# Kernel tuning notes

Measured on AMD Instinct MI355X. Metric: run time of the kernel, lower is better.

Reference implementation:

```python
import jax, jax.numpy as jnp
import numpy as np

DIM = 512
NUM_HEADS = 8
HEAD_DIM = DIM // NUM_HEADS
B, S = 2, 2048


def setup_inputs() -> dict:
    key = jax.random.key(0)
    ks = jax.random.split(key, 16)
    scale = 1.0 / np.sqrt(DIM)
    inp = {
        "x": jax.random.normal(ks[0], (B, S, DIM), dtype=jnp.float32),
        "Qexpl": jax.random.normal(ks[1], (B, S, DIM), dtype=jnp.float32),
        "Kexpl": jax.random.normal(ks[2], (B, S, DIM), dtype=jnp.float32),
        "fl": jax.random.uniform(ks[3], (B,), dtype=jnp.float32),
        "fu": jax.random.uniform(ks[4], (B,), dtype=jnp.float32),
        "age": jax.random.uniform(ks[5], (B,), dtype=jnp.float32),
        "gender": jax.random.uniform(ks[6], (B,), dtype=jnp.float32),
        # Linear params: weight stored as [out, in] like torch; y = x @ W.T + b
        "Wq": jax.random.normal(ks[7], (DIM, DIM), dtype=jnp.float32) * scale,
        "bq": jnp.zeros((DIM,), dtype=jnp.float32),
        "Wk": jax.random.normal(ks[8], (DIM, DIM), dtype=jnp.float32) * scale,
        "bk": jnp.zeros((DIM,), dtype=jnp.float32),
        "Wv": jax.random.normal(ks[9], (DIM, DIM), dtype=jnp.float32) * scale,
        "bv": jnp.zeros((DIM,), dtype=jnp.float32),
        "Wo": jax.random.normal(ks[10], (DIM, DIM), dtype=jnp.float32) * scale,
        "bo": jnp.zeros((DIM,), dtype=jnp.float32),
    }
    return inp


def reference(x, Qexpl, Kexpl, fl, fu, age, gender, Wq, bq, Wk, bk, Wv, bv, Wo, bo):
    # drofe_fn is None -> Q/K projections used directly.
    Q = Qexpl @ Wq.T + bq            # [B, S, D]
    K = Kexpl @ Wk.T + bk            # [B, S, D]
    V = x @ Wv.T + bv                # [B, S, D]

    def split_heads(t):  # [B, S, D] -> [B, H, S, hd]
        return t.reshape(B, S, NUM_HEADS, HEAD_DIM).transpose(0, 2, 1, 3)

    Qh, Kh, Vh = split_heads(Q), split_heads(K), split_heads(V)
    scale = 1.0 / np.sqrt(HEAD_DIM).astype(np.float32)
    scores = jnp.einsum("bhqd,bhkd->bhqk", Qh, Kh) * scale  # [B, H, S, S]
    weights = jax.nn.softmax(scores, axis=-1)
    attn = jnp.einsum("bhqk,bhkd->bhqd", weights, Vh)        # [B, H, S, hd]
    attn = attn.transpose(0, 2, 1, 3).reshape(B, S, DIM)
    return attn @ Wo.T + bo
```

## Files before the change

### kernel.cpp

```cpp
#include <hip/hip_runtime.h>
#include <hip/hip_bf16.h>

typedef unsigned short ushort_t;
typedef __attribute__((ext_vector_type(8))) short bf16x8;
typedef __attribute__((ext_vector_type(4))) float f32x4;

__device__ __forceinline__ ushort_t f2bf(float f) {
    union { float f; unsigned u; } v; v.f = f;
    unsigned r = v.u + 0x7FFF + ((v.u >> 16) & 1);
    return (ushort_t)(r >> 16);
}
__device__ __forceinline__ float bfl(ushort_t u) {
    union { unsigned u; float f; } v; v.u = (unsigned)u << 16; return v.f;
}
__device__ __forceinline__ bf16x8 ld8(const ushort_t* p) { return *(const bf16x8*)p; }

__device__ __forceinline__ unsigned cvt2(float x, float y) {
    __hip_bfloat162 h = __float22bfloat162_rn(make_float2(x, y));
    unsigned r; __builtin_memcpy(&r, &h, 4); return r;
}
__device__ __forceinline__ bf16x8 pack8f(float4 a, float4 b) {
    union { unsigned u[4]; bf16x8 v; } o;
    o.u[0] = cvt2(a.x, a.y); o.u[1] = cvt2(a.z, a.w);
    o.u[2] = cvt2(b.x, b.y); o.u[3] = cvt2(b.z, b.w);
    return o.v;
}

__device__ __forceinline__ void gload_lds16(const ushort_t* g, ushort_t* l) {
    __builtin_amdgcn_global_load_lds(
        (const __attribute__((address_space(1))) void*)g,
        (__attribute__((address_space(3))) void*)l, 16, 0, 0);
}

__global__ __launch_bounds__(256)
void cast_kernel(const float* __restrict__ Qe, const float* __restrict__ Ke,
                 const float* __restrict__ x,  const float* __restrict__ Wq,
                 const float* __restrict__ Wk, const float* __restrict__ Wv,
                 const float* __restrict__ Wo,
                 ushort_t* __restrict__ Ab, ushort_t* __restrict__ Wb)
{
    const unsigned i8 = (blockIdx.x * 256u + threadIdx.x) * 8u;
    const float* src; ushort_t* dst;
    if (i8 < (3u << 21)) {
        unsigned a = i8 >> 21, off = i8 & ((1u << 21) - 1);
        src = (a == 0 ? Qe : a == 1 ? Ke : x) + off;
        dst = Ab + i8;
    } else {
        unsigned j = i8 - (3u << 21);
        unsigned a = j >> 18, off = j & ((1u << 18) - 1);
        src = (a == 0 ? Wq : a == 1 ? Wk : a == 2 ? Wv : Wo) + off;
        dst = Wb + j;
    }
    *(bf16x8*)dst = pack8f(*(const float4*)src, *(const float4*)(src + 4));
}

__global__ __launch_bounds__(256, 2)
void proj_qkv_kernel(const ushort_t* __restrict__ Ab, const ushort_t* __restrict__ Wb,
                     const float* __restrict__ bq, const float* __restrict__ bk,
                     const float* __restrict__ bv,
                     ushort_t* __restrict__ Qo, ushort_t* __restrict__ Ko,
                     ushort_t* __restrict__ Vt)
{
    __shared__ ushort_t smem[4 * 128 * 64];

    const int z = blockIdx.z;
    const ushort_t* A = Ab + ((size_t)z << 21);
    const ushort_t* W = Wb + ((size_t)z << 18);
    const float* bias = (z == 0) ? bq : (z == 1) ? bk : bv;

    const int m0 = blockIdx.y * 128, n0 = blockIdx.x * 128;
    const int t = threadIdx.x;
    const int lane = t & 63, wave = t >> 6;
    const int wm = (wave & 1) * 64, wn = (wave >> 1) * 64;
    const int fr = lane & 15, quad = lane >> 4;
    const int fr7 = fr & 7;

    const int srl = wave * 32 + (lane >> 3);
    const int sch = ((lane & 7) ^ (srl & 7)) << 3;
    const ushort_t* ag = A + (size_t)(m0 + srl) * 512 + sch;
    const ushort_t* wg = W + (size_t)(n0 + srl) * 512 + sch;
    const int dbase = wave * 32 * 64;

    f32x4 acc[4][4] = {};

#pragma unroll
    for (int i = 0; i < 4; ++i)
        gload_lds16(ag + (size_t)(i * 8) * 512, smem + dbase + i * 512);
#pragma unroll
    for (int i = 0; i < 4; ++i)
        gload_lds16(wg + (size_t)(i * 8) * 512, smem + 8192 + dbase + i * 512);
    __syncthreads();

    for (int kk = 0; kk < 8; ++kk) {
        ushort_t* cur = smem + ((kk & 1) << 14);
        ushort_t* nxt = smem + (((kk & 1) ^ 1) << 14);
        if (kk < 7) {
            int ko = (kk + 1) * 64;
#pragma unroll
            for (int i = 0; i < 4; ++i)
                gload_lds16(ag + ko + (size_t)(i * 8) * 512, nxt + dbase + i * 512);
#pragma unroll
            for (int i = 0; i < 4; ++i)
                gload_lds16(wg + ko + (size_t)(i * 8) * 512, nxt + 8192 + dbase + i * 512);
        }

#pragma unroll
        for (int ks = 0; ks < 2; ++ks) {
            bf16x8 af[4], bfr[4];
#pragma unroll
            for (int mt = 0; mt < 4; ++mt)
                af[mt] = ld8(cur + (wm + mt * 16 + fr) * 64 + (((ks * 4 + quad) ^ fr7) << 3));
#pragma unroll
            for (int nt = 0; nt < 4; ++nt)
                bfr[nt] = ld8(cur + 8192 + (wn + nt * 16 + fr) * 64 + (((ks * 4 + quad) ^ fr7) << 3));
#pragma unroll
            for (int mt = 0; mt < 4; ++mt)
#pragma unroll
                for (int nt = 0; nt < 4; ++nt)
                    acc[mt][nt] = __builtin_amdgcn_mfma_f32_16x16x32_bf16(
                        af[mt], bfr[nt], acc[mt][nt], 0, 0, 0);
        }
        asm volatile("s_waitcnt vmcnt(0)" ::: "memory");
        __builtin_amdgcn_s_barrier();
        __builtin_amdgcn_sched_barrier(0);
    }

    const float C1 = 0.125f * 1.44269504088896340736f;
    if (z != 2) {
        ushort_t* dst = (z == 0) ? Qo : Ko;
#pragma unroll
        for (int nt = 0; nt < 4; ++nt) {
            int n = n0 + wn + nt * 16 + fr;
            float bb = bias[n];
#pragma unroll
            for (int mt = 0; mt < 4; ++mt) {
                int mb = m0 + wm + mt * 16 + quad * 4;
                if (z == 0) {
#pragma unroll
                    for (int r = 0; r < 4; ++r)
                        dst[(size_t)(mb + r) * 512 + n] = f2bf((acc[mt][nt][r] + bb) * C1);
                } else {
#pragma unroll
                    for (int r = 0; r < 4; ++r)
                        dst[(size_t)(mb + r) * 512 + n] = f2bf(acc[mt][nt][r] + bb);
                }
            }
        }
    } else {
        ushort_t* lT = smem;
#pragma unroll
        for (int nt = 0; nt < 4; ++nt) {
            int nl = wn + nt * 16 + fr;
            float bb = bias[n0 + nl];
#pragma unroll
            for (int mt = 0; mt < 4; ++mt) {
                int tm = wm + mt * 16 + quad * 4;
#pragma unroll
                for (int r = 0; r < 4; ++r) {
                    int tl = tm + r;
                    int sg = (tl & 96) + ((tl & 12) << 1) + ((tl >> 4 & 1) << 2) + (tl & 3);
                    lT[nl * 136 + sg] = f2bf(acc[mt][nt][r] + bb);
                }
            }
        }
        __syncthreads();
        const int bidx = m0 >> 11, m0t = m0 & 2047;
#pragma unroll
        for (int i = 0; i < 8; ++i) {
            int s = i * 256 + t;
            int row = s >> 4, c = s & 15;
            int n = n0 + row;
            int h = n >> 6, d = n & 63;
            bf16x8 v = ld8(lT + row * 136 + c * 8);
            *(bf16x8*)(Vt + ((size_t)((bidx * 8 + h) * 64 + d)) * 2048 + m0t + c * 8) = v;
        }
    }
}

__global__ __launch_bounds__(256, 2)
void gemm_o_kernel(const ushort_t* __restrict__ Oh, const float* __restrict__ Lsum,
                   const ushort_t* __restrict__ W, const float* __restrict__ bias,
                   float* __restrict__ dst)
{
    __shared__ ushort_t lA[64 * 72];
    __shared__ ushort_t lB[64 * 72];
    const int m0 = blockIdx.y * 64, n0 = blockIdx.x * 64;
    const int t = threadIdx.x;
    const int lane = t & 63, wave = t >> 6;
    const int wm = (wave & 1) * 32, wn = (wave >> 1) * 32;
    const int fr = lane & 15, quad = lane >> 4;
    const int bq_ = m0 >> 11, qq0 = m0 & 2047;

    f32x4 acc[2][2] = {};
    bf16x8 va0[2], va1[2], vw[2];
    float l0[2], l1[2];

#pragma unroll
    for (int i = 0; i < 2; ++i) {
        int s = i * 256 + t;
        int r = s >> 3, jp = s & 7;
        va0[i] = ld8(Oh + (size_t)(m0 + r) * 512 + jp * 8);
        va1[i] = ld8(Oh + (size_t)(m0 + r + 4096) * 512 + jp * 8);
        l0[i] = Lsum[(bq_ * 8 + 0) * 2048 + qq0 + r];
        l1[i] = Lsum[((2 + bq_) * 8 + 0) * 2048 + qq0 + r];
        vw[i] = ld8(W + (size_t)(n0 + r) * 512 + jp * 8);
    }

    for (int kk = 0; kk < 8; ++kk) {
        if (kk) __syncthreads();
#pragma unroll
        for (int i = 0; i < 2; ++i) {
            int s = i * 256 + t;
            int r = s >> 3, jp = s & 7;
            float inv = 1.f / (l0[i] + l1[i]);
            union { bf16x8 v; ushort_t s8[8]; } a0, a1;
            a0.v = va0[i]; a1.v = va1[i];
            union { unsigned u[4]; bf16x8 v; } o;
#pragma unroll
            for (int j = 0; j < 4; ++j)
                o.u[j] = cvt2((bfl(a0.s8[2 * j]) + bfl(a1.s8[2 * j])) * inv,
                              (bfl(a0.s8[2 * j + 1]) + bfl(a1.s8[2 * j + 1])) * inv);
            *(bf16x8*)(lA + r * 72 + jp * 8) = o.v;
            *(bf16x8*)(lB + r * 72 + jp * 8) = vw[i];
        }
        __syncthreads();
        if (kk < 7) {
            int k0 = (kk + 1) * 64;
#pragma unroll
            for (int i = 0; i < 2; ++i) {
                int s = i * 256 + t;
                int r = s >> 3, jp = s & 7;
                va0[i] = ld8(Oh + (size_t)(m0 + r) * 512 + k0 + jp * 8);
                va1[i] = ld8(Oh + (size_t)(m0 + r + 4096) * 512 + k0 + jp * 8);
                l0[i] = Lsum[(bq_ * 8 + kk + 1) * 2048 + qq0 + r];
                l1[i] = Lsum[((2 + bq_) * 8 + kk + 1) * 2048 + qq0 + r];
                vw[i] = ld8(W + (size_t)(n0 + r) * 512 + k0 + jp * 8);
            }
        }

        bf16x8 af[2][2], bfrag[2][2];
#pragma unroll
        for (int ks = 0; ks < 2; ++ks) {
#pragma unroll
            for (int mt = 0; mt < 2; ++mt)
                af[mt][ks] = ld8(lA + (wm + mt * 16 + fr) * 72 + (ks * 4 + quad) * 8);
#pragma unroll
            for (int nt = 0; nt < 2; ++nt)
                bfrag[nt][ks] = ld8(lB + (wn + nt * 16 + fr) * 72 + (ks * 4 + quad) * 8);
        }
#pragma unroll
        for (int ks = 0; ks < 2; ++ks)
#pragma unroll
            for (int mt = 0; mt < 2; ++mt)
#pragma unroll
                for (int nt = 0; nt < 2; ++nt)
                    acc[mt][nt] = __builtin_amdgcn_mfma_f32_16x16x32_bf16(
                        af[mt][ks], bfrag[nt][ks], acc[mt][nt], 0, 0, 0);
    }

#pragma unroll
    for (int nt = 0; nt < 2; ++nt) {
        int n = n0 + wn + nt * 16 + fr;
        float bb = bias[n];
#pragma unroll
        for (int mt = 0; mt < 2; ++mt) {
            int mb = m0 + wm + mt * 16 + quad * 4;
#pragma unroll
            for (int r = 0; r < 4; ++r)
                dst[(size_t)(mb + r) * 512 + n] = acc[mt][nt][r] + bb;
        }
    }
}

__global__ __launch_bounds__(256, 4)
void attn_kernel(const ushort_t* __restrict__ Q, const ushort_t* __restrict__ K,
                 const ushort_t* __restrict__ Vt, ushort_t* __restrict__ Opart,
                 float* __restrict__ Lsum)
{
    __shared__ ushort_t lK[128 * 64];
    __shared__ ushort_t lV[64 * 128];

    const int b = blockIdx.z >> 1, half = blockIdx.z & 1;
    const int h = blockIdx.y;
    const int q0 = blockIdx.x * 64;
    const int kvbase = half * 1024;
    const int t = threadIdx.x;
    const int lane = t & 63, w = t >> 6;
    const int wq = w * 16;
    const int fr = lane & 15, quad = lane >> 4;
    const int fr7 = fr & 7;

    bf16x8 aq[2];
    {
        const ushort_t* qp = Q + (size_t)(b * 2048 + q0 + wq + fr) * 512 + h * 64 + quad * 8;
        aq[0] = ld8(qp);
        aq[1] = ld8(qp + 32);
    }

    const int krl = w * 32 + (lane >> 3);
    const ushort_t* kg = K + (size_t)(b * 2048 + kvbase + krl) * 512 + h * 64
                           + (lane & 7) * 8;
    ushort_t* lk_wr = lK + krl * 64 + (((lane & 7) ^ (krl & 7)) << 3);

    const int vrl = w * 4 + (lane >> 4);
    const ushort_t* vbase = Vt + (size_t)((b * 8 + h) * 64 + vrl) * 2048 + kvbase
                              + (((lane & 15) ^ (vrl & 7)) << 3);

    const ushort_t* kr0 = lK + fr * 64 + ((quad ^ fr7) << 3);
    const ushort_t* kr1 = lK + fr * 64 + (((4 + quad) ^ fr7) << 3);
    const ushort_t* vr0 = lV + fr * 128 + (((0 * 4 + quad) ^ fr7) << 3);
    const ushort_t* vr1 = lV + fr * 128 + (((1 * 4 + quad) ^ fr7) << 3);
    const ushort_t* vr2 = lV + fr * 128 + (((2 * 4 + quad) ^ fr7) << 3);
    const ushort_t* vr3 = lV + fr * 128 + (((3 * 4 + quad) ^ fr7) << 3);
    const ushort_t* vr[4] = { vr0, vr1, vr2, vr3 };

    bf16x8 kreg[4];
#pragma unroll
    for (int i = 0; i < 4; ++i)
        kreg[i] = ld8(kg + (size_t)(i * 8) * 512);
#pragma unroll
    for (int i = 0; i < 4; ++i)
        *(bf16x8*)(lk_wr + i * 8 * 64) = kreg[i];
    __syncthreads();

    f32x4 oacc[4] = {};
    float lsum = 0.f;

    for (int tt = 0; tt < 8; ++tt) {
        const int kv = tt << 7;

#pragma unroll
        for (int i = 0; i < 4; ++i)
            gload_lds16(vbase + kv + (size_t)(i * 16) * 2048, lV + (i * 16 + w * 4) * 128);
        __builtin_amdgcn_sched_barrier(0);
        if (tt < 7) {
#pragma unroll
            for (int i = 0; i < 4; ++i)
                kreg[i] = ld8(kg + (size_t)(kv + 128 + i * 8) * 512);
        }
        __builtin_amdgcn_sched_barrier(0);

        f32x4 sc[8] = {};
        __builtin_amdgcn_s_setprio(1);
#pragma unroll
        for (int nt = 0; nt < 8; ++nt) {
            bf16x8 kb = ld8(kr0 + nt * 16 * 64);
            sc[nt] = __builtin_amdgcn_mfma_f32_16x16x32_bf16(kb, aq[0], sc[nt], 0, 0, 0);
        }
#pragma unroll
        for (int nt = 0; nt < 8; ++nt) {
            bf16x8 kb = ld8(kr1 + nt * 16 * 64);
            sc[nt] = __builtin_amdgcn_mfma_f32_16x16x32_bf16(kb, aq[1], sc[nt], 0, 0, 0);
        }
        __builtin_amdgcn_s_setprio(0);

        if (tt < 7) asm volatile("s_waitcnt vmcnt(4)" ::: "memory");
        else        asm volatile("s_waitcnt vmcnt(0)" ::: "memory");
        __builtin_amdgcn_s_barrier();
        __builtin_amdgcn_sched_barrier(0);

        __builtin_amdgcn_s_setprio(1);
#pragma unroll
        for (int ks = 0; ks < 4; ++ks) {
            float p0[4], p1[4];
#pragma unroll
            for (int r = 0; r < 4; ++r) p0[r] = exp2f(sc[2 * ks][r]);
#pragma unroll
            for (int r = 0; r < 4; ++r) p1[r] = exp2f(sc[2 * ks + 1][r]);
            lsum += ((p0[0] + p0[1]) + (p0[2] + p0[3]))
                  + ((p1[0] + p1[1]) + (p1[2] + p1[3]));
            union { unsigned u[4]; bf16x8 v; } pa;
            pa.u[0] = cvt2(p0[0], p0[1]); pa.u[1] = cvt2(p0[2], p0[3]);
            pa.u[2] = cvt2(p1[0], p1[1]); pa.u[3] = cvt2(p1[2], p1[3]);
#pragma unroll
            for (int nt = 0; nt < 4; ++nt) {
                bf16x8 vb = ld8(vr[ks] + nt * 16 * 128);
                oacc[nt] = __builtin_amdgcn_mfma_f32_16x16x32_bf16(pa.v, vb, oacc[nt], 0, 0, 0);
            }
            if (ks == 0 && tt < 7) {
#pragma unroll
                for (int i = 0; i < 4; ++i)
                    *(bf16x8*)(lk_wr + i * 8 * 64) = kreg[i];
            }
        }
        __builtin_amdgcn_s_setprio(0);
        __syncthreads();
    }

    float rs = lsum;
    rs += __shfl_xor(rs, 16, 64);
    rs += __shfl_xor(rs, 32, 64);
#pragma unroll
    for (int r = 0; r < 4; ++r) {
        int qrow = q0 + wq + quad * 4 + r;
        ushort_t* od = Opart + ((size_t)(half * 2 + b) * 2048 + qrow) * 512 + h * 64;
#pragma unroll
        for (int nt = 0; nt < 4; ++nt)
            od[nt * 16 + fr] = f2bf(oacc[nt][r]);
    }
    if (lane < 16)
        Lsum[((half * 2 + b) * 8 + h) * 2048 + q0 + wq + lane] = rs;
}

extern "C" void kernel_launch(void* const* d_in, const int* in_sizes, int n_in,
                              void* d_out, int out_size, void* d_ws, size_t ws_size,
                              hipStream_t stream) {
    const float* x   = (const float*)d_in[0];
    const float* Qe  = (const float*)d_in[1];
    const float* Ke  = (const float*)d_in[2];
    const float* Wq  = (const float*)d_in[7];
    const float* bq  = (const float*)d_in[8];
    const float* Wk  = (const float*)d_in[9];
    const float* bk  = (const float*)d_in[10];
    const float* Wv  = (const float*)d_in[11];
    const float* bv  = (const float*)d_in[12];
    const float* Wo  = (const float*)d_in[13];
    const float* bo  = (const float*)d_in[14];

    const size_t NTOK = 2 * 2048;
    const size_t ACT = NTOK * 512;

    ushort_t* p = (ushort_t*)d_ws;
    ushort_t* Abf = p; p += (size_t)3 << 21;
    ushort_t* Wbf = p; p += (size_t)4 << 18;
    ushort_t* Qws = p; p += ACT;
    ushort_t* Kws = p; p += ACT;
    ushort_t* Vt  = p; p += ACT;
    ushort_t* OpH = p; p += 2 * ACT;
    float* Lsum  = (float*)p;

    cast_kernel<<<dim3(3584), 256, 0, stream>>>(Qe, Ke, x, Wq, Wk, Wv, Wo, Abf, Wbf);
    proj_qkv_kernel<<<dim3(4, 32, 3), 256, 0, stream>>>(Abf, Wbf, bq, bk, bv,
                                                        Qws, Kws, Vt);
    attn_kernel<<<dim3(32, 8, 4), 256, 0, stream>>>(Qws, Kws, Vt, OpH, Lsum);
    gemm_o_kernel<<<dim3(8, 64), 256, 0, stream>>>(OpH, Lsum, Wbf + ((size_t)3 << 18),
                                                   bo, (float*)d_out);
}
```

Measured before the change: 157.1 us.

## Shrink QKV projection N-tile and compute softmax row sums via MFMA ones column

The QKV projection tile narrows from 128 to 64 columns, doubling the grid and raising the occupancy target to 3 blocks per CU, which should fill more CUs for this small GEMM. In attention, the per-row exp sum is no longer accumulated with scalar adds and cross-lane shuffles. Instead a 16-row block of bf16 ones is appended to the V tile in LDS, so one extra MFMA per k-step produces the row sums. This trades VALU adds for extra matrix work and rounds the sum through bf16 probabilities, and the added LDS may affect attention occupancy.

```diff
diff --git a/kernel.cpp b/kernel.cpp
--- a/kernel.cpp
+++ b/kernel.cpp
@@ -54,69 +54,72 @@
     *(bf16x8*)dst = pack8f(*(const float4*)src, *(const float4*)(src + 4));
 }
 
-__global__ __launch_bounds__(256, 2)
+__global__ __launch_bounds__(256, 3)
 void proj_qkv_kernel(const ushort_t* __restrict__ Ab, const ushort_t* __restrict__ Wb,
                      const float* __restrict__ bq, const float* __restrict__ bk,
                      const float* __restrict__ bv,
                      ushort_t* __restrict__ Qo, ushort_t* __restrict__ Ko,
                      ushort_t* __restrict__ Vt)
 {
-    __shared__ ushort_t smem[4 * 128 * 64];
+    __shared__ ushort_t smem[2 * (128 + 64) * 64];
 
     const int z = blockIdx.z;
     const ushort_t* A = Ab + ((size_t)z << 21);
     const ushort_t* W = Wb + ((size_t)z << 18);
     const float* bias = (z == 0) ? bq : (z == 1) ? bk : bv;
 
-    const int m0 = blockIdx.y * 128, n0 = blockIdx.x * 128;
+    const int m0 = blockIdx.y * 128, n0 = blockIdx.x * 64;
     const int t = threadIdx.x;
     const int lane = t & 63, wave = t >> 6;
-    const int wm = (wave & 1) * 64, wn = (wave >> 1) * 64;
+    const int wm = (wave & 1) * 64, wn = (wave >> 1) * 32;
     const int fr = lane & 15, quad = lane >> 4;
     const int fr7 = fr & 7;
 
     const int srl = wave * 32 + (lane >> 3);
     const int sch = ((lane & 7) ^ (srl & 7)) << 3;
     const ushort_t* ag = A + (size_t)(m0 + srl) * 512 + sch;
-    const ushort_t* wg = W + (size_t)(n0 + srl) * 512 + sch;
-    const int dbase = wave * 32 * 64;
-
-    f32x4 acc[4][4] = {};
+    const int dbA = wave * 32 * 64;
+    const int swl = wave * 16 + (lane >> 3);
+    const int schw = ((lane & 7) ^ (swl & 7)) << 3;
+    const ushort_t* wg = W + (size_t)(n0 + swl) * 512 + schw;
+    const int dbW = wave * 16 * 64;
+
+    f32x4 acc[4][2] = {};
 
 #pragma unroll
     for (int i = 0; i < 4; ++i)
-        gload_lds16(ag + (size_t)(i * 8) * 512, smem + dbase + i * 512);
-#pragma unroll
-    for (int i = 0; i < 4; ++i)
-        gload_lds16(wg + (size_t)(i * 8) * 512, smem + 8192 + dbase + i * 512);
+        gload_lds16(ag + (size_t)(i * 8) * 512, smem + dbA + i * 512);
+#pragma unroll
+    for (int i = 0; i < 2; ++i)
+        gload_lds16(wg + (size_t)(i * 8) * 512, smem + 8192 + dbW + i * 512);
     __syncthreads();
 
     for (int kk = 0; kk < 8; ++kk) {
-        ushort_t* cur = smem + ((kk & 1) << 14);
-        ushort_t* nxt = smem + (((kk & 1) ^ 1) << 14);
+        ushort_t* cur = smem + (kk & 1) * 12288;
+        ushort_t* nxt = smem + ((kk & 1) ^ 1) * 12288;
         if (kk < 7) {
             int ko = (kk + 1) * 64;
 #pragma unroll
             for (int i = 0; i < 4; ++i)
-                gload_lds16(ag + ko + (size_t)(i * 8) * 512, nxt + dbase + i * 512);
-#pragma unroll
-            for (int i = 0; i < 4; ++i)
-                gload_lds16(wg + ko + (size_t)(i * 8) * 512, nxt + 8192 + dbase + i * 512);
+                gload_lds16(ag + ko + (size_t)(i * 8) * 512, nxt + dbA + i * 512);
+#pragma unroll
+            for (int i = 0; i < 2; ++i)
+                gload_lds16(wg + ko + (size_t)(i * 8) * 512, nxt + 8192 + dbW + i * 512);
         }
 
 #pragma unroll
         for (int ks = 0; ks < 2; ++ks) {
-            bf16x8 af[4], bfr[4];
+            bf16x8 af[4], bfr[2];
 #pragma unroll
             for (int mt = 0; mt < 4; ++mt)
                 af[mt] = ld8(cur + (wm + mt * 16 + fr) * 64 + (((ks * 4 + quad) ^ fr7) << 3));
 #pragma unroll
-            for (int nt = 0; nt < 4; ++nt)
+            for (int nt = 0; nt < 2; ++nt)
                 bfr[nt] = ld8(cur + 8192 + (wn + nt * 16 + fr) * 64 + (((ks * 4 + quad) ^ fr7) << 3));
 #pragma unroll
             for (int mt = 0; mt < 4; ++mt)
 #pragma unroll
-                for (int nt = 0; nt < 4; ++nt)
+                for (int nt = 0; nt < 2; ++nt)
                     acc[mt][nt] = __builtin_amdgcn_mfma_f32_16x16x32_bf16(
                         af[mt], bfr[nt], acc[mt][nt], 0, 0, 0);
         }
@@ -129,7 +132,7 @@
     if (z != 2) {
         ushort_t* dst = (z == 0) ? Qo : Ko;
 #pragma unroll
-        for (int nt = 0; nt < 4; ++nt) {
+        for (int nt = 0; nt < 2; ++nt) {
             int n = n0 + wn + nt * 16 + fr;
             float bb = bias[n];
 #pragma unroll
@@ -149,7 +152,7 @@
     } else {
         ushort_t* lT = smem;
 #pragma unroll
-        for (int nt = 0; nt < 4; ++nt) {
+        for (int nt = 0; nt < 2; ++nt) {
             int nl = wn + nt * 16 + fr;
             float bb = bias[n0 + nl];
 #pragma unroll
@@ -166,7 +169,7 @@
         __syncthreads();
         const int bidx = m0 >> 11, m0t = m0 & 2047;
 #pragma unroll
-        for (int i = 0; i < 8; ++i) {
+        for (int i = 0; i < 4; ++i) {
             int s = i * 256 + t;
             int row = s >> 4, c = s & 15;
             int n = n0 + row;
@@ -278,7 +281,7 @@
                  float* __restrict__ Lsum)
 {
     __shared__ ushort_t lK[128 * 64];
-    __shared__ ushort_t lV[64 * 128];
+    __shared__ ushort_t lV[80 * 128];
 
     const int b = blockIdx.z >> 1, half = blockIdx.z & 1;
     const int h = blockIdx.y;
@@ -314,6 +317,12 @@
     const ushort_t* vr3 = lV + fr * 128 + (((3 * 4 + quad) ^ fr7) << 3);
     const ushort_t* vr[4] = { vr0, vr1, vr2, vr3 };
 
+    if (t < 16) {
+        union { unsigned u[4]; bf16x8 v; } one;
+        one.u[0] = one.u[1] = one.u[2] = one.u[3] = 0x3F803F80u;
+        *(bf16x8*)(lV + 64 * 128 + t * 8) = one.v;
+    }
+
     bf16x8 kreg[4];
 #pragma unroll
     for (int i = 0; i < 4; ++i)
@@ -323,8 +332,7 @@
         *(bf16x8*)(lk_wr + i * 8 * 64) = kreg[i];
     __syncthreads();
 
-    f32x4 oacc[4] = {};
-    float lsum = 0.f;
+    f32x4 oacc[5] = {};
 
     for (int tt = 0; tt < 8; ++tt) {
         const int kv = tt << 7;
@@ -367,13 +375,11 @@
             for (int r = 0; r < 4; ++r) p0[r] = exp2f(sc[2 * ks][r]);
 #pragma unroll
             for (int r = 0; r < 4; ++r) p1[r] = exp2f(sc[2 * ks + 1][r]);
-            lsum += ((p0[0] + p0[1]) + (p0[2] + p0[3]))
-                  + ((p1[0] + p1[1]) + (p1[2] + p1[3]));
             union { unsigned u[4]; bf16x8 v; } pa;
             pa.u[0] = cvt2(p0[0], p0[1]); pa.u[1] = cvt2(p0[2], p0[3]);
             pa.u[2] = cvt2(p1[0], p1[1]); pa.u[3] = cvt2(p1[2], p1[3]);
 #pragma unroll
-            for (int nt = 0; nt < 4; ++nt) {
+            for (int nt = 0; nt < 5; ++nt) {
                 bf16x8 vb = ld8(vr[ks] + nt * 16 * 128);
                 oacc[nt] = __builtin_amdgcn_mfma_f32_16x16x32_bf16(pa.v, vb, oacc[nt], 0, 0, 0);
             }
@@ -387,9 +393,6 @@
         __syncthreads();
     }
 
-    float rs = lsum;
-    rs += __shfl_xor(rs, 16, 64);
-    rs += __shfl_xor(rs, 32, 64);
 #pragma unroll
     for (int r = 0; r < 4; ++r) {
         int qrow = q0 + wq + quad * 4 + r;
@@ -398,8 +401,12 @@
         for (int nt = 0; nt < 4; ++nt)
             od[nt * 16 + fr] = f2bf(oacc[nt][r]);
     }
-    if (lane < 16)
-        Lsum[((half * 2 + b) * 8 + h) * 2048 + q0 + wq + lane] = rs;
+    if (fr == 0) {
+        int base = ((half * 2 + b) * 8 + h) * 2048 + q0 + wq + quad * 4;
+#pragma unroll
+        for (int r = 0; r < 4; ++r)
+            Lsum[base + r] = oacc[4][r];
+    }
 }
 
 extern "C" void kernel_launch(void* const* d_in, const int* in_sizes, int n_in,
@@ -430,7 +437,7 @@
     float* Lsum  = (float*)p;
 
     cast_kernel<<<dim3(3584), 256, 0, stream>>>(Qe, Ke, x, Wq, Wk, Wv, Wo, Abf, Wbf);
-    proj_qkv_kernel<<<dim3(4, 32, 3), 256, 0, stream>>>(Abf, Wbf, bq, bk, bv,
+    proj_qkv_kernel<<<dim3(8, 32, 3), 256, 0, stream>>>(Abf, Wbf, bq, bk, bv,
                                                         Qws, Kws, Vt);
     attn_kernel<<<dim3(32, 8, 4), 256, 0, stream>>>(Qws, Kws, Vt, OpH, Lsum);
     gemm_o_kernel<<<dim3(8, 64), 256, 0, stream>>>(OpH, Lsum, Wbf + ((size_t)3 << 18),
```

New measurement: 160.1 us. About the same (+1.9%).
